# Kernel tuning notes

Measured on AMD Instinct MI355X. Metric: run time of the kernel, lower is better.

## Reference

```python
import jax, jax.numpy as jnp
import numpy as np

INPUT_DIM = 1024
EMBED_DIM = 256


def setup_inputs() -> dict:
    key = jax.random.key(0)
    ks = jax.random.split(key, 7)
    s_in = 1.0 / np.sqrt(INPUT_DIM)
    x = jax.random.normal(ks[0], (4, 2048, INPUT_DIM), dtype=jnp.float32)
    Wq = jax.random.uniform(ks[1], (INPUT_DIM, EMBED_DIM), jnp.float32, -s_in, s_in)
    bq = jax.random.uniform(ks[2], (EMBED_DIM,), jnp.float32, -s_in, s_in)
    Wk = jax.random.uniform(ks[3], (INPUT_DIM, EMBED_DIM), jnp.float32, -s_in, s_in)
    bk = jax.random.uniform(ks[4], (EMBED_DIM,), jnp.float32, -s_in, s_in)
    Wv = jax.random.uniform(ks[5], (INPUT_DIM, EMBED_DIM), jnp.float32, -s_in, s_in)
    bv = jax.random.uniform(ks[6], (EMBED_DIM,), jnp.float32, -s_in, s_in)
    return {"x": x, "Wq": Wq, "bq": bq, "Wk": Wk, "bk": bk, "Wv": Wv, "bv": bv}


def reference(x, Wq, bq, Wk, bk, Wv, bv):
    # B,T,C -> single-head attention. NOTE: original multiplies by C**0.5.
    C = x.shape[-1]
    scale = jnp.asarray(C, x.dtype) ** 0.5
    q = jnp.einsum('btc,ce->bte', x, Wq) + bq  # [B,T,E]
    k = jnp.einsum('btc,ce->bte', x, Wk) + bk
    v = jnp.einsum('btc,ce->bte', x, Wv) + bv
    wei = jnp.einsum('bqe,bke->bqk', q, k) * scale  # [B,T,T]
    wei = jax.nn.softmax(wei, axis=-1)
    # dropout p=0.0 (eval): identity
    out = jnp.einsum('bqk,bke->bqe', wei, v)  # [B,T,E]
    return out
```

## Files before the change

kernel.cpp:

```cpp
#include <hip/hip_runtime.h>
#include <math.h>

#define IDIM 1024
#define EDIM 256
#define NB 4
#define NT 2048
#define NROW 8192

typedef __attribute__((ext_vector_type(8))) short short8;
typedef __attribute__((ext_vector_type(4))) float f32x4;

#define MFMA16(A,B,C) __builtin_amdgcn_mfma_f32_16x16x32_bf16(A,B,C,0,0,0)
#define GLD16(gsrc, ldst) __builtin_amdgcn_global_load_lds( \
    (const __attribute__((address_space(1))) unsigned int*)(gsrc), \
    (__attribute__((address_space(3))) unsigned int*)(ldst), 16, 0, 0)

#define WAITV4() asm volatile("s_waitcnt vmcnt(4)" ::: "memory")
#define WAITV0() asm volatile("s_waitcnt vmcnt(0)" ::: "memory")
#define BAR() do { asm volatile("" ::: "memory"); __builtin_amdgcn_s_barrier(); \
                   asm volatile("" ::: "memory"); } while (0)

__device__ __forceinline__ unsigned short f2bf(float x){
    unsigned u = __builtin_bit_cast(unsigned, x);
    u += 0x7fffu + ((u >> 16) & 1u);
    return (unsigned short)(u >> 16);
}
__device__ __forceinline__ float bf2f(unsigned short h){
    unsigned u = ((unsigned)h) << 16;
    return __builtin_bit_cast(float, u);
}

__global__ __launch_bounds__(256) void split_w(
    const float* __restrict__ Wq, const float* __restrict__ Wk, const float* __restrict__ Wv,
    ushort* __restrict__ Wqh, ushort* __restrict__ Wql,
    ushort* __restrict__ Wkh, ushort* __restrict__ Wkl,
    ushort* __restrict__ Wvh)
{
    int u = blockIdx.x * 256 + threadIdx.x;
    int z   = u >> 15;
    int rem = u & 32767;
    int ko  = rem >> 8;
    int e   = rem & 255;
    const float* W = (z == 0) ? Wq : (z == 1) ? Wk : Wv;
    ushort* Oh = (z == 0) ? Wqh : (z == 1) ? Wkh : Wvh;
    ushort* Ol = (z == 0) ? Wql : Wkl;
    union { ushort us[8]; uint4 v; } hi, lo;
    #pragma unroll
    for (int j = 0; j < 8; ++j) {
        float wv = W[(size_t)(ko * 8 + j) * 256 + e];
        unsigned short h = f2bf(wv);
        hi.us[j] = h;
        lo.us[j] = f2bf(wv - bf2f(h));
    }
    *(uint4*)(Oh + (size_t)e * 1024 + ko * 8) = hi.v;
    if (z < 2) *(uint4*)(Ol + (size_t)e * 1024 + ko * 8) = lo.v;
}

__global__ __launch_bounds__(256, 3) void qkv_proj(
    const float* __restrict__ X,
    const ushort* __restrict__ Whq, const ushort* __restrict__ Wlq,
    const ushort* __restrict__ Whk, const ushort* __restrict__ Wlk,
    const ushort* __restrict__ Whv,
    const float* __restrict__ bq, const float* __restrict__ bk, const float* __restrict__ bv,
    ushort* __restrict__ Qh, ushort* __restrict__ Ql,
    ushort* __restrict__ Kh, ushort* __restrict__ Kl,
    ushort* __restrict__ Vt)
{
    __shared__ ushort Ah[259 * 8], Al[259 * 8];
    __shared__ ushort Bh[512 * 8], Bl[512 * 8];

    const int tid = threadIdx.x;
    const int lane = tid & 63, w = tid >> 6;
    const int ln = tid & 15, quad = (tid >> 4) & 3;
    const int z = blockIdx.z;
    const int n0 = blockIdx.x * 128, m0 = blockIdx.y * 64;
    const ushort* Wh = (z == 0) ? Whq : (z == 1) ? Whk : Whv;
    const ushort* Wl = (z == 0) ? Wlq : Wlk;

    f32x4 acc[4][2];
    #pragma unroll
    for (int mi = 0; mi < 4; ++mi)
        #pragma unroll
        for (int ni = 0; ni < 2; ++ni) acc[mi][ni] = (f32x4){0.f, 0.f, 0.f, 0.f};

    const int am = tid >> 2, ak8 = (tid & 3) * 8;
    const float* xp = X + (size_t)(m0 + am) * IDIM + ak8;
    const ushort* bsrc0 = Wh + (size_t)(n0 + lane) * IDIM + w * 8;
    const ushort* bsrc1 = Wh + (size_t)(n0 + 64 + lane) * IDIM + w * 8;
    const ushort* blsrc0 = Wl + (size_t)(n0 + lane) * IDIM + w * 8;
    const ushort* blsrc1 = Wl + (size_t)(n0 + 64 + lane) * IDIM + w * 8;
    ushort* bd0 = Bh + (size_t)(w * 128) * 8;
    ushort* bd1 = Bh + (size_t)(w * 128 + 64) * 8;
    ushort* bld0 = Bl + (size_t)(w * 128) * 8;
    ushort* bld1 = Bl + (size_t)(w * 128 + 64) * 8;

    for (int kk = 0; kk < IDIM; kk += 32) {
        GLD16(bsrc0 + kk, bd0);
        GLD16(bsrc1 + kk, bd1);
        if (z < 2) { GLD16(blsrc0 + kk, bld0); GLD16(blsrc1 + kk, bld1); }
        {
            float4 a0 = *(const float4*)(xp + kk);
            float4 a1 = *(const float4*)(xp + kk + 4);
            float xv[8] = {a0.x, a0.y, a0.z, a0.w, a1.x, a1.y, a1.z, a1.w};
            union { ushort us[8]; uint4 v; } hi, lo;
            #pragma unroll
            for (int j = 0; j < 8; ++j) {
                unsigned short hh = f2bf(xv[j]);
                hi.us[j] = hh;
                lo.us[j] = f2bf(xv[j] - bf2f(hh));
            }
            int unit = (tid & 3) * 65 + am;
            *(uint4*)(Ah + unit * 8) = hi.v;
            if (z < 2) *(uint4*)(Al + unit * 8) = lo.v;
        }
        __syncthreads();

        short8 ah[4], al4[4];
        #pragma unroll
        for (int mi = 0; mi < 4; ++mi) {
            int au = quad * 65 + mi * 16 + ln;
            ah[mi] = *(const short8*)(Ah + au * 8);
            if (z < 2) al4[mi] = *(const short8*)(Al + au * 8);
        }
        #pragma unroll
        for (int ni = 0; ni < 2; ++ni) {
            int bu = quad * 128 + w * 32 + ni * 16 + ln;
            short8 bh = *(const short8*)(Bh + bu * 8);
            if (z < 2) {
                short8 bl = *(const short8*)(Bl + bu * 8);
                #pragma unroll
                for (int mi = 0; mi < 4; ++mi) {
                    acc[mi][ni] = MFMA16(ah[mi], bh, acc[mi][ni]);
                    acc[mi][ni] = MFMA16(ah[mi], bl, acc[mi][ni]);
                    acc[mi][ni] = MFMA16(al4[mi], bh, acc[mi][ni]);
                }
            } else {
                #pragma unroll
                for (int mi = 0; mi < 4; ++mi)
                    acc[mi][ni] = MFMA16(ah[mi], bh, acc[mi][ni]);
            }
        }
        __syncthreads();
    }

    if (z < 2) {
        ushort* OH = (z == 0) ? Qh : Kh;
        ushort* OL = (z == 0) ? Ql : Kl;
        const float* bias = (z == 0) ? bq : bk;
        const float scale = (z == 0) ? 46.16624130844683f : 1.0f;
        #pragma unroll
        for (int ni = 0; ni < 2; ++ni) {
            int col = n0 + w * 32 + ni * 16 + ln;
            float bb = bias[col];
            #pragma unroll
            for (int mi = 0; mi < 4; ++mi)
                #pragma unroll
                for (int r = 0; r < 4; ++r) {
                    int row = m0 + mi * 16 + quad * 4 + r;
                    float v = (acc[mi][ni][r] + bb) * scale;
                    unsigned short hh = f2bf(v);
                    OH[(size_t)row * EDIM + col] = hh;
                    OL[(size_t)row * EDIM + col] = f2bf(v - bf2f(hh));
                }
        }
    } else {
        #pragma unroll
        for (int ni = 0; ni < 2; ++ni) {
            int col = n0 + w * 32 + ni * 16 + ln;
            float bb = bv[col];
            #pragma unroll
            for (int mi = 0; mi < 4; ++mi) {
                int rowb = m0 + mi * 16 + quad * 4;
                union { ushort us[4]; uint2 v; } pk;
                #pragma unroll
                for (int r = 0; r < 4; ++r) pk.us[r] = f2bf(acc[mi][ni][r] + bb);
                *(uint2*)(Vt + (size_t)col * NROW + rowb) = pk.v;
            }
        }
    }
}


__device__ __forceinline__ void stageK(const ushort* __restrict__ Kh,
                                       const ushort* __restrict__ Kl,
                                       ushort* buf, int kv0, int kc0, int w, int lane) {
    size_t rowoff = (size_t)(kv0 + w * 16 + (lane & 15)) * EDIM + (lane >> 4) * 8 + kc0 * 32;
    GLD16(Kh + rowoff,      buf + w * 512);
    GLD16(Kh + rowoff + 32, buf + 2048 + w * 512);
    GLD16(Kl + rowoff,      buf + 4096 + w * 512);
    GLD16(Kl + rowoff + 32, buf + 6144 + w * 512);
}

__device__ __forceinline__ void stageV(const ushort* __restrict__ Vt,
                                       ushort* buf, int kv0, int vs0, int w, int lane) {
    size_t gv = (size_t)(vs0 * 64 + w * 16 + (lane & 15)) * NROW + kv0 + (lane >> 4) * 8;
    GLD16(Vt + gv,      buf + w * 1024);
    GLD16(Vt + gv + 32, buf + w * 1024 + 512);
    GLD16(Vt + gv + (size_t)64 * NROW,      buf + 4096 + w * 1024);
    GLD16(Vt + gv + (size_t)64 * NROW + 32, buf + 4096 + w * 1024 + 512);
}

__global__ __launch_bounds__(256, 2) void attn(
    const ushort* __restrict__ Qh, const ushort* __restrict__ Ql,
    const ushort* __restrict__ Kh, const ushort* __restrict__ Kl,
    const ushort* __restrict__ Vt, ushort* __restrict__ Op, float* __restrict__ mlbuf)
{
    __shared__ ushort KVbuf[3 * 8192];
    __shared__ ushort Pall[4 * 1088];

    const int tid = threadIdx.x;
    const int lane = tid & 63;
    const int ln = tid & 15, quad = (tid >> 4) & 3, w = tid >> 6;
    ushort* Pw = Pall + w * 1088;

    const int id = blockIdx.x;
    const int cls = id & 15;
    const int b = cls >> 2, kvq = cls & 3;
    const int qt = id >> 4;
    const int qrow0w = b * NT + qt * 64 + w * 16;
    const int kvbase = b * NT + kvq * 512;

    short8 qh8[8], ql8[8];
    #pragma unroll
    for (int kc = 0; kc < 8; ++kc) {
        qh8[kc] = *(const short8*)(Qh + (size_t)(qrow0w + ln) * EDIM + kc * 32 + quad * 8);
        ql8[kc] = *(const short8*)(Ql + (size_t)(qrow0w + ln) * EDIM + kc * 32 + quad * 8);
    }

    float m_r[4], l_r[4];
    #pragma unroll
    for (int r = 0; r < 4; ++r) { m_r[r] = -3e38f; l_r[r] = 0.f; }
    f32x4 o[16];
    #pragma unroll
    for (int ni = 0; ni < 16; ++ni) o[ni] = (f32x4){0.f, 0.f, 0.f, 0.f};

    stageK(Kh, Kl, KVbuf + 0 * 8192, kvbase, 0, w, lane);
    stageK(Kh, Kl, KVbuf + 1 * 8192, kvbase, 2, w, lane);

    #pragma unroll 1
    for (int t = 0; t < 8; ++t) {
        const int kv0 = kvbase + t * 64;
        f32x4 s[4];
        #pragma unroll
        for (int ni = 0; ni < 4; ++ni) s[ni] = (f32x4){0.f, 0.f, 0.f, 0.f};

        #pragma unroll
        for (int j = 0; j < 4; ++j) {
            WAITV4();
            BAR();
            if (j < 2)      stageK(Kh, Kl, KVbuf + ((j + 2) % 3) * 8192, kv0, 2 * (j + 2), w, lane);
            else if (j == 2) stageV(Vt, KVbuf + 1 * 8192, kv0, 0, w, lane);
            else             stageV(Vt, KVbuf + 2 * 8192, kv0, 2, w, lane);

            const ushort* bufc = KVbuf + (j % 3) * 8192;
            #pragma unroll
            for (int kk = 0; kk < 2; ++kk) {
                const int kc = j * 2 + kk;
                #pragma unroll
                for (int ni = 0; ni < 4; ++ni) {
                    short8 bh = *(const short8*)(bufc + kk * 2048 + (ni * 64 + quad * 16 + ln) * 8);
                    short8 bl = *(const short8*)(bufc + 4096 + kk * 2048 + (ni * 64 + quad * 16 + ln) * 8);
                    s[ni] = MFMA16(qh8[kc], bh, s[ni]);
                    s[ni] = MFMA16(qh8[kc], bl, s[ni]);
                    s[ni] = MFMA16(ql8[kc], bh, s[ni]);
                }
            }
        }

        float mt[4];
        #pragma unroll
        for (int r = 0; r < 4; ++r)
            mt[r] = fmaxf(fmaxf(s[0][r], s[1][r]), fmaxf(s[2][r], s[3][r]));
        #pragma unroll
        for (int mask = 1; mask < 16; mask <<= 1)
            #pragma unroll
            for (int r = 0; r < 4; ++r)
                mt[r] = fmaxf(mt[r], __shfl_xor(mt[r], mask));
        float alpha[4];
        #pragma unroll
        for (int r = 0; r < 4; ++r) {
            float mn = fmaxf(m_r[r], mt[r]);
            alpha[r] = exp2f(m_r[r] - mn);
            m_r[r] = mn;
        }
        float ls[4] = {0.f, 0.f, 0.f, 0.f};
        #pragma unroll
        for (int ni = 0; ni < 4; ++ni) {
            int colb = ni * 16 + ln;
            #pragma unroll
            for (int r = 0; r < 4; ++r) {
                float p = exp2f(s[ni][r] - m_r[r]);
                ls[r] += p;
                Pw[((colb >> 3) * 17 + quad * 4 + r) * 8 + (colb & 7)] = f2bf(p);
            }
        }
        #pragma unroll
        for (int mask = 1; mask < 16; mask <<= 1)
            #pragma unroll
            for (int r = 0; r < 4; ++r)
                ls[r] += __shfl_xor(ls[r], mask);
        #pragma unroll
        for (int r = 0; r < 4; ++r) l_r[r] = l_r[r] * alpha[r] + ls[r];
        #pragma unroll
        for (int ni = 0; ni < 16; ++ni)
            #pragma unroll
            for (int r = 0; r < 4; ++r) o[ni][r] *= alpha[r];

        short8 apk0 = *(const short8*)(Pw + (quad * 17 + ln) * 8);
        short8 apk1 = *(const short8*)(Pw + ((4 + quad) * 17 + ln) * 8);

        #pragma unroll
        for (int j2 = 0; j2 < 2; ++j2) {
            if (t < 7 || j2 == 0) { WAITV4(); } else { WAITV0(); }
            BAR();
            if (t < 7) {
                if (j2 == 0) stageK(Kh, Kl, KVbuf + 0 * 8192, kv0 + 64, 0, w, lane);
                else         stageK(Kh, Kl, KVbuf + 1 * 8192, kv0 + 64, 2, w, lane);
            }
            const ushort* bufc = KVbuf + (1 + j2) * 8192;
            #pragma unroll
            for (int vv = 0; vv < 2; ++vv) {
                const int vs = j2 * 2 + vv;
                #pragma unroll
                for (int ni = 0; ni < 4; ++ni) {
                    short8 v0 = *(const short8*)(bufc + vv * 4096 + (ni * 128 + quad * 16 + ln) * 8);
                    short8 v1 = *(const short8*)(bufc + vv * 4096 + (ni * 128 + 64 + quad * 16 + ln) * 8);
                    o[vs * 4 + ni] = MFMA16(apk0, v0, o[vs * 4 + ni]);
                    o[vs * 4 + ni] = MFMA16(apk1, v1, o[vs * 4 + ni]);
                }
            }
        }
    }

    const int p = (b * 32 + qt) * 4 + kvq;
    if (ln == 0) {
        #pragma unroll
        for (int r = 0; r < 4; ++r) {
            int row = w * 16 + quad * 4 + r;
            *(float2*)(mlbuf + ((size_t)p * 64 + row) * 2) = make_float2(m_r[r], l_r[r]);
        }
    }
    #pragma unroll
    for (int ni = 0; ni < 16; ++ni)
        #pragma unroll
        for (int r = 0; r < 4; ++r) {
            int row = w * 16 + quad * 4 + r;
            Op[(size_t)p * 16384 + row * 256 + ni * 16 + ln] = f2bf(o[ni][r]);
        }
}

__global__ __launch_bounds__(256) void attn_merge(
    const ushort* __restrict__ Op, const float* __restrict__ mlbuf, float* __restrict__ out)
{
    const int bid = blockIdx.x, t = threadIdx.x;
    const int b = bid >> 7, qt = (bid >> 2) & 31, rg = bid & 3;
    const int row = rg * 16 + (t >> 4);
    const int e0 = (t & 15) * 16;
    const int pb = (b * 32 + qt) * 4;
    float mv[4], lv[4];
    float M = -3e38f;
    #pragma unroll
    for (int w2 = 0; w2 < 4; ++w2) {
        float2 ml = *(const float2*)(mlbuf + ((size_t)(pb + w2) * 64 + row) * 2);
        mv[w2] = ml.x; lv[w2] = ml.y;
        M = fmaxf(M, ml.x);
    }
    float sc[4], denom = 0.f;
    #pragma unroll
    for (int w2 = 0; w2 < 4; ++w2) {
        sc[w2] = exp2f(mv[w2] - M);
        denom += sc[w2] * lv[w2];
    }
    float inv = 1.0f / denom;
    #pragma unroll
    for (int w2 = 0; w2 < 4; ++w2) sc[w2] *= inv;

    float acc[16] = {};
    #pragma unroll
    for (int w2 = 0; w2 < 4; ++w2) {
        const ushort* src = Op + (size_t)(pb + w2) * 16384 + row * 256 + e0;
        #pragma unroll
        for (int c = 0; c < 2; ++c) {
            union { ushort us[8]; uint4 v; } u;
            u.v = *(const uint4*)(src + c * 8);
            #pragma unroll
            for (int j = 0; j < 8; ++j)
                acc[c * 8 + j] += sc[w2] * bf2f(u.us[j]);
        }
    }
    float* op = out + ((size_t)b * NT + qt * 64 + row) * EDIM + e0;
    #pragma unroll
    for (int g = 0; g < 4; ++g)
        *(float4*)(op + g * 4) = make_float4(acc[g*4], acc[g*4+1], acc[g*4+2], acc[g*4+3]);
}

extern "C" void kernel_launch(void* const* d_in, const int* in_sizes, int n_in,
                              void* d_out, int out_size, void* d_ws, size_t ws_size,
                              hipStream_t stream) {
    const float* x  = (const float*)d_in[0];
    const float* Wq = (const float*)d_in[1];
    const float* bq = (const float*)d_in[2];
    const float* Wk = (const float*)d_in[3];
    const float* bk = (const float*)d_in[4];
    const float* Wv = (const float*)d_in[5];
    const float* bv = (const float*)d_in[6];
    float* out = (float*)d_out;

    const size_t NE = (size_t)NB * NT * EDIM;
    ushort* Qh = (ushort*)d_ws;
    ushort* Ql = Qh + NE;
    ushort* Kh = Ql + NE;
    ushort* Kl = Kh + NE;
    ushort* Vt = Kl + NE;
    ushort* Wqh = Vt + NE;
    ushort* Wql = Wqh + 256 * 1024;
    ushort* Wkh = Wql + 256 * 1024;
    ushort* Wkl = Wkh + 256 * 1024;
    ushort* Wvh = Wkl + 256 * 1024;
    ushort* Op  = Wvh + 256 * 1024;
    float*  mlb = (float*)(Op + (size_t)512 * 16384);

    split_w<<<384, 256, 0, stream>>>(Wq, Wk, Wv, Wqh, Wql, Wkh, Wkl, Wvh);
    qkv_proj<<<dim3(2, 128, 3), 256, 0, stream>>>(x, Wqh, Wql, Wkh, Wkl, Wvh,
                                                  bq, bk, bv, Qh, Ql, Kh, Kl, Vt);
    attn<<<512, 256, 0, stream>>>(Qh, Ql, Kh, Kl, Vt, Op, mlb);
    attn_merge<<<512, 256, 0, stream>>>(Op, mlb, out);
}
```

Baseline: 206.1 us.

## Load V directly from global into registers and deepen K LDS pipeline

V tiles for the PV matmul are now loaded by each wave directly from global memory into registers, no longer staged through shared memory, so the V-phase barriers are removed. The freed LDS schedule becomes a four-buffer K ring with three chunks in flight, and the wait counts are adjusted to match. This cuts LDS traffic and barriers in the PV phase. In exchange it adds register pressure (32 short8 values for V), uses more LDS, and puts uncoalesced global load latency on the critical path.

```diff
diff --git a/kernel.cpp b/kernel.cpp
--- a/kernel.cpp
+++ b/kernel.cpp
@@ -15,6 +15,7 @@
     (const __attribute__((address_space(1))) unsigned int*)(gsrc), \
     (__attribute__((address_space(3))) unsigned int*)(ldst), 16, 0, 0)
 
+#define WAITV8() asm volatile("s_waitcnt vmcnt(8)" ::: "memory")
 #define WAITV4() asm volatile("s_waitcnt vmcnt(4)" ::: "memory")
 #define WAITV0() asm volatile("s_waitcnt vmcnt(0)" ::: "memory")
 #define BAR() do { asm volatile("" ::: "memory"); __builtin_amdgcn_s_barrier(); \
@@ -183,21 +184,12 @@
 
 __device__ __forceinline__ void stageK(const ushort* __restrict__ Kh,
                                        const ushort* __restrict__ Kl,
-                                       ushort* buf, int kv0, int kc0, int w, int lane) {
-    size_t rowoff = (size_t)(kv0 + w * 16 + (lane & 15)) * EDIM + (lane >> 4) * 8 + kc0 * 32;
+                                       ushort* buf, int kvrow0, int kc0, int w, int lane) {
+    size_t rowoff = (size_t)(kvrow0 + w * 16 + (lane & 15)) * EDIM + (lane >> 4) * 8 + kc0 * 32;
     GLD16(Kh + rowoff,      buf + w * 512);
     GLD16(Kh + rowoff + 32, buf + 2048 + w * 512);
     GLD16(Kl + rowoff,      buf + 4096 + w * 512);
     GLD16(Kl + rowoff + 32, buf + 6144 + w * 512);
-}
-
-__device__ __forceinline__ void stageV(const ushort* __restrict__ Vt,
-                                       ushort* buf, int kv0, int vs0, int w, int lane) {
-    size_t gv = (size_t)(vs0 * 64 + w * 16 + (lane & 15)) * NROW + kv0 + (lane >> 4) * 8;
-    GLD16(Vt + gv,      buf + w * 1024);
-    GLD16(Vt + gv + 32, buf + w * 1024 + 512);
-    GLD16(Vt + gv + (size_t)64 * NROW,      buf + 4096 + w * 1024);
-    GLD16(Vt + gv + (size_t)64 * NROW + 32, buf + 4096 + w * 1024 + 512);
 }
 
 __global__ __launch_bounds__(256, 2) void attn(
@@ -205,7 +197,7 @@
     const ushort* __restrict__ Kh, const ushort* __restrict__ Kl,
     const ushort* __restrict__ Vt, ushort* __restrict__ Op, float* __restrict__ mlbuf)
 {
-    __shared__ ushort KVbuf[3 * 8192];
+    __shared__ ushort KVbuf[4 * 8192];
     __shared__ ushort Pall[4 * 1088];
 
     const int tid = threadIdx.x;
@@ -236,6 +228,7 @@
 
     stageK(Kh, Kl, KVbuf + 0 * 8192, kvbase, 0, w, lane);
     stageK(Kh, Kl, KVbuf + 1 * 8192, kvbase, 2, w, lane);
+    stageK(Kh, Kl, KVbuf + 2 * 8192, kvbase, 4, w, lane);
 
     #pragma unroll 1
     for (int t = 0; t < 8; ++t) {
@@ -246,13 +239,19 @@
 
         #pragma unroll
         for (int j = 0; j < 4; ++j) {
-            WAITV4();
+            if (t == 7 && j == 2)      { WAITV4(); }
+            else if (t == 7 && j == 3) { WAITV0(); }
+            else                       { WAITV8(); }
             BAR();
-            if (j < 2)      stageK(Kh, Kl, KVbuf + ((j + 2) % 3) * 8192, kv0, 2 * (j + 2), w, lane);
-            else if (j == 2) stageV(Vt, KVbuf + 1 * 8192, kv0, 0, w, lane);
-            else             stageV(Vt, KVbuf + 2 * 8192, kv0, 2, w, lane);
-
-            const ushort* bufc = KVbuf + (j % 3) * 8192;
+            if (t < 7) {
+                if (j == 0)      stageK(Kh, Kl, KVbuf + 3 * 8192, kv0,      6, w, lane);
+                else if (j == 1) stageK(Kh, Kl, KVbuf + 0 * 8192, kv0 + 64, 0, w, lane);
+                else if (j == 2) stageK(Kh, Kl, KVbuf + 1 * 8192, kv0 + 64, 2, w, lane);
+                else             stageK(Kh, Kl, KVbuf + 2 * 8192, kv0 + 64, 4, w, lane);
+            } else if (j == 0) {
+                stageK(Kh, Kl, KVbuf + 3 * 8192, kv0, 6, w, lane);
+            }
+            const ushort* bufc = KVbuf + j * 8192;
             #pragma unroll
             for (int kk = 0; kk < 2; ++kk) {
                 const int kc = j * 2 + kk;
@@ -267,6 +266,16 @@
             }
         }
 
+        short8 vg0[8], vg1[8];
+        #pragma unroll
+        for (int f = 0; f < 8; ++f) {
+            const int c2 = f >> 2, ni = f & 3;
+            vg0[f] = *(const short8*)(Vt + (size_t)((0 * 4 + ni) * 16 + ln) * NROW
+                                         + kv0 + c2 * 32 + quad * 8);
+            vg1[f] = *(const short8*)(Vt + (size_t)((1 * 4 + ni) * 16 + ln) * NROW
+                                         + kv0 + c2 * 32 + quad * 8);
+        }
+
         float mt[4];
         #pragma unroll
         for (int r = 0; r < 4; ++r)
@@ -310,25 +319,36 @@
         short8 apk1 = *(const short8*)(Pw + ((4 + quad) * 17 + ln) * 8);
 
         #pragma unroll
-        for (int j2 = 0; j2 < 2; ++j2) {
-            if (t < 7 || j2 == 0) { WAITV4(); } else { WAITV0(); }
-            BAR();
-            if (t < 7) {
-                if (j2 == 0) stageK(Kh, Kl, KVbuf + 0 * 8192, kv0 + 64, 0, w, lane);
-                else         stageK(Kh, Kl, KVbuf + 1 * 8192, kv0 + 64, 2, w, lane);
-            }
-            const ushort* bufc = KVbuf + (1 + j2) * 8192;
-            #pragma unroll
-            for (int vv = 0; vv < 2; ++vv) {
-                const int vs = j2 * 2 + vv;
-                #pragma unroll
-                for (int ni = 0; ni < 4; ++ni) {
-                    short8 v0 = *(const short8*)(bufc + vv * 4096 + (ni * 128 + quad * 16 + ln) * 8);
-                    short8 v1 = *(const short8*)(bufc + vv * 4096 + (ni * 128 + 64 + quad * 16 + ln) * 8);
-                    o[vs * 4 + ni] = MFMA16(apk0, v0, o[vs * 4 + ni]);
-                    o[vs * 4 + ni] = MFMA16(apk1, v1, o[vs * 4 + ni]);
-                }
-            }
+        for (int ni = 0; ni < 4; ++ni) {
+            o[0 + ni] = MFMA16(apk0, vg0[ni], o[0 + ni]);
+            o[0 + ni] = MFMA16(apk1, vg0[4 + ni], o[0 + ni]);
+        }
+        #pragma unroll
+        for (int f = 0; f < 8; ++f) {
+            const int c2 = f >> 2, ni = f & 3;
+            vg0[f] = *(const short8*)(Vt + (size_t)((2 * 4 + ni) * 16 + ln) * NROW
+                                         + kv0 + c2 * 32 + quad * 8);
+        }
+        #pragma unroll
+        for (int ni = 0; ni < 4; ++ni) {
+            o[4 + ni] = MFMA16(apk0, vg1[ni], o[4 + ni]);
+            o[4 + ni] = MFMA16(apk1, vg1[4 + ni], o[4 + ni]);
+        }
+        #pragma unroll
+        for (int f = 0; f < 8; ++f) {
+            const int c2 = f >> 2, ni = f & 3;
+            vg1[f] = *(const short8*)(Vt + (size_t)((3 * 4 + ni) * 16 + ln) * NROW
+                                         + kv0 + c2 * 32 + quad * 8);
+        }
+        #pragma unroll
+        for (int ni = 0; ni < 4; ++ni) {
+            o[8 + ni] = MFMA16(apk0, vg0[ni], o[8 + ni]);
+            o[8 + ni] = MFMA16(apk1, vg0[4 + ni], o[8 + ni]);
+        }
+        #pragma unroll
+        for (int ni = 0; ni < 4; ++ni) {
+            o[12 + ni] = MFMA16(apk0, vg1[ni], o[12 + ni]);
+            o[12 + ni] = MFMA16(apk1, vg1[4 + ni], o[12 + ni]);
         }
     }
 
```

New measurement: 239.4 us. 16.1% more time.
